# Kernel tuning notes

Hardware: AMD Instinct MI355X
Metric: run time of the kernel (lower is better)

The kernel has to match this reference:

```python
import jax, jax.numpy as jnp
import numpy as np

N_TRAIN, DIM, OUT_DIM, BATCH = 16384, 64, 8, 8192


def setup_inputs() -> dict:
    key = jax.random.key(0)
    k1, k2, k3 = jax.random.split(key, 3)
    batches = jax.random.uniform(k1, (BATCH, DIM), dtype=jnp.float32)
    x_training = jax.random.uniform(k2, (N_TRAIN, DIM), dtype=jnp.float32)
    y_training = jax.random.normal(k3, (N_TRAIN, OUT_DIM), dtype=jnp.float32)
    beta = jnp.ones((1, N_TRAIN), dtype=jnp.float32) / 0.1  # matches ones/0.1 init
    return {"batches": batches, "x_training": x_training,
            "y_training": y_training, "beta": beta}


def reference(batches, x_training, y_training, beta):
    # Pairwise Euclidean distances [batch, n_train] via the expanded form
    # (avoids the O(batch*n_train*dim) repeated tensor the torch code builds).
    b2 = jnp.sum(batches * batches, axis=1, keepdims=True)        # [B, 1]
    x2 = jnp.sum(x_training * x_training, axis=1)[None, :]        # [1, N]
    sq = jnp.maximum(b2 + x2 - 2.0 * (batches @ x_training.T), 0.0)
    dist = jnp.sqrt(sq)                                           # [B, N]
    radial_val = jnp.exp(-beta * dist)                            # RBF kernel [B, N]
    psum1 = jnp.sum(radial_val, axis=1, keepdims=True)            # [B, 1]
    psum2 = radial_val @ y_training                               # [B, OUT_DIM]
    return psum2 / psum1
```

## Files before the change

kernel.cpp:

```cpp
#include <hip/hip_runtime.h>
#include <math.h>
#include <stdint.h>

#define NTRAIN 16384
#define DIM 64
#define ODIM 8
#define BATCH 8192
#define LOG2E 1.4426950408889634f

typedef float f32x16 __attribute__((ext_vector_type(16)));
typedef short short8 __attribute__((ext_vector_type(8)));
typedef _Float16 f16x8 __attribute__((ext_vector_type(8)));
typedef unsigned short u16;

static __device__ __forceinline__ u16 f2bf(float f) {
  unsigned u = __builtin_bit_cast(unsigned, f);
  u += 0x7FFFu + ((u >> 16) & 1u);
  return (u16)(u >> 16);
}
static __device__ __forceinline__ u16 f2h(float f) {
  return __builtin_bit_cast(u16, (_Float16)f);
}
static __device__ __forceinline__ float h2f(u16 h) {
  return (float)__builtin_bit_cast(_Float16, h);
}

static __device__ __forceinline__ f32x16 mfma_bf(short8 a, short8 b, f32x16 c) {
  return __builtin_amdgcn_mfma_f32_32x32x16_bf16(a, b, c, 0, 0, 0);
}
static __device__ __forceinline__ f32x16 mfma_h(f16x8 a, f16x8 b, f32x16 c) {
  return __builtin_amdgcn_mfma_f32_32x32x16_f16(a, b, c, 0, 0, 0);
}
static __device__ __forceinline__ unsigned pkbf(float a, float b) {
  unsigned d;
  asm("v_cvt_pk_bf16_f32 %0, %1, %2" : "=v"(d) : "v"(a), "v"(b));
  return d;
}
static __device__ __forceinline__ float ex2n(float x) {
  float r;
  asm("v_exp_f32 %0, -%1" : "=v"(r) : "v"(x));
  return r;
}
static __device__ __forceinline__ void plswap(unsigned& a, unsigned& b) {
  asm("v_permlane32_swap_b32 %0, %1" : "+v"(a), "+v"(b));
}

__global__ __launch_bounds__(256) void k_norm(
    const float* __restrict__ batches, const float* __restrict__ xt,
    float* __restrict__ b2, float* __restrict__ x2) {
  int i = blockIdx.x * 256 + threadIdx.x;
  if (i >= BATCH + NTRAIN) return;
  const float* row = (i < BATCH) ? batches + (size_t)i * DIM
                                 : xt + (size_t)(i - BATCH) * DIM;
  const float4* r4 = (const float4*)row;
  float s0 = 0.f, s1 = 0.f, s2 = 0.f, s3 = 0.f;
#pragma unroll
  for (int q = 0; q < DIM / 4; ++q) {
    float4 v = r4[q];
    s0 = fmaf(v.x, v.x, s0); s1 = fmaf(v.y, v.y, s1);
    s2 = fmaf(v.z, v.z, s2); s3 = fmaf(v.w, v.w, s3);
  }
  float nrm = (s0 + s1) + (s2 + s3);
  if (i < BATCH) b2[i] = nrm;
  else x2[i - BATCH] = nrm;
}

__global__ __launch_bounds__(256) void k_frag(
    const float* __restrict__ xt, const float* __restrict__ yt,
    const float* __restrict__ beta, const float* __restrict__ x2,
    u16* __restrict__ xf, u16* __restrict__ yv) {
  int tid = blockIdx.x * 256 + threadIdx.x;

  if (tid < (NTRAIN / 32) * 5 * 64) {
    int fg = tid >> 6, lane = tid & 63;
    int tile = fg / 5, f = fg % 5;
    int lr = lane & 31, hi = lane >> 5;
    uint4 u = {0, 0, 0, 0};
    if (f == 4) {
      if (hi == 0) {
        int n = tile * 32 + lr;
        float g = beta[n] * LOG2E;
        float g2v = g * g;
        float gx2v = g2v * x2[n];
        u16 xh = f2h(gx2v);
        u16 xl = f2h(gx2v - h2f(xh));
        u16 gh = f2h(g2v);
        u16 gl = f2h(g2v - h2f(gh));
        u.x = (unsigned)xh | ((unsigned)xl << 16);
        u.y = (unsigned)gh | ((unsigned)gh << 16);
        u.z = (unsigned)gl;
      }
    } else {
      int n = tile * 32 + lr;
      float g = beta[n] * LOG2E;
      float s2g = 2.0f * g * g;
      const float* src = xt + (size_t)n * DIM + f * 16 + hi * 8;
      unsigned e[8];
#pragma unroll
      for (int j = 0; j < 8; ++j) e[j] = f2h(s2g * src[j]);
      u.x = e[0] | (e[1] << 16); u.y = e[2] | (e[3] << 16);
      u.z = e[4] | (e[5] << 16); u.w = e[6] | (e[7] << 16);
    }
    ((uint4*)xf)[(size_t)fg * 64 + lane] = u;
    return;
  }
  tid -= (NTRAIN / 32) * 5 * 64;

  if (tid < (NTRAIN / 16) * 64) {
    int frag = tid >> 6, lane = tid & 63;
    int col = lane & 31, hi = lane >> 5;
    int n = frag * 16 + hi * 8;
    unsigned e[8];
#pragma unroll
    for (int j = 0; j < 8; ++j) {
      float v = (col == 0) ? 1.0f : ((col < 9) ? yt[(size_t)(n + j) * ODIM + (col - 1)] : 0.0f);
      e[j] = f2bf(v);
    }
    uint4 u;
    u.x = e[0] | (e[1] << 16); u.y = e[2] | (e[3] << 16);
    u.z = e[4] | (e[5] << 16); u.w = e[6] | (e[7] << 16);
    ((uint4*)yv)[(size_t)frag * 64 + lane] = u;
  }
}

#define LOAD5(X_, nbv)                                                        \
  {                                                                           \
    const size_t fb_ = (size_t)((nbv) >> 5) * 5;                              \
    _Pragma("unroll")                                                         \
    for (int f = 0; f < 5; ++f) X_[f] = xf4[(fb_ + f) * 64 + lane];           \
  }

#define COMPUTE(X_, nbv)                                                      \
  {                                                                           \
    short8 V0 = __builtin_bit_cast(short8,                                    \
                                   yv4[(size_t)((nbv) >> 4) * 64 + lane]);    \
    short8 V1 = __builtin_bit_cast(                                           \
        short8, yv4[(size_t)((nbv) >> 4) * 64 + 64 + lane]);                  \
    f32x16 sA;                                                                \
    _Pragma("unroll")                                                         \
    for (int r = 0; r < 16; ++r) sA[r] = 0.f;                                 \
    __builtin_amdgcn_s_setprio(1);                                            \
    sA = mfma_h(__builtin_bit_cast(f16x8, X_[4]), AN, sA);                    \
    _Pragma("unroll")                                                         \
    for (int ks = 0; ks < 4; ++ks)                                            \
      sA = mfma_h(__builtin_bit_cast(f16x8, X_[ks]), AH[ks], sA);             \
    __builtin_amdgcn_s_setprio(0);                                            \
    unsigned U[8];                                                            \
    _Pragma("unroll")                                                         \
    for (int p = 0; p < 8; ++p) {                                             \
      float d0 = __builtin_amdgcn_sqrtf(fabsf(sA[2 * p]));                    \
      float d1 = __builtin_amdgcn_sqrtf(fabsf(sA[2 * p + 1]));                \
      U[p] = pkbf(ex2n(d0), ex2n(d1));                                        \
    }                                                                         \
    plswap(U[0], U[2]); plswap(U[1], U[3]);                                   \
    plswap(U[4], U[6]); plswap(U[5], U[7]);                                   \
    uint4 a1 = {U[0], U[1], U[2], U[3]};                                      \
    uint4 a2 = {U[4], U[5], U[6], U[7]};                                      \
    pv = mfma_bf(__builtin_bit_cast(short8, a1), V0, pv);                     \
    pv = mfma_bf(__builtin_bit_cast(short8, a2), V1, pv);                     \
  }

__global__ __launch_bounds__(256, 4) void grnn_pass1(
    const u16* __restrict__ xf, const u16* __restrict__ yv,
    const float* __restrict__ batches, const float* __restrict__ b2,
    float* __restrict__ partial, int chunk_n) {
  const int lane = threadIdx.x & 63;
  const int lr = lane & 31, hi = lane >> 5;
  const int mrow0 = blockIdx.x * 128 + (threadIdx.x >> 6) * 32;
  const int c = blockIdx.y;
  const int n0 = c * chunk_n;
  const int nslab = chunk_n / 32;

  f16x8 AH[4], AN;
  const int mrow = mrow0 + lr;
#pragma unroll
  for (int ks = 0; ks < 4; ++ks) {
    const float* src = batches + (size_t)mrow * DIM + ks * 16 + hi * 8;
    float4 v0 = *(const float4*)src;
    float4 v1 = *(const float4*)(src + 4);
    AH[ks][0] = (_Float16)v0.x; AH[ks][1] = (_Float16)v0.y;
    AH[ks][2] = (_Float16)v0.z; AH[ks][3] = (_Float16)v0.w;
    AH[ks][4] = (_Float16)v1.x; AH[ks][5] = (_Float16)v1.y;
    AH[ks][6] = (_Float16)v1.z; AH[ks][7] = (_Float16)v1.w;
  }
#pragma unroll
  for (int j = 0; j < 8; ++j) AN[j] = (_Float16)0.0f;
  if (hi == 0) {
    float b2v = b2[mrow];
    _Float16 bh = (_Float16)b2v;
    _Float16 bl = (_Float16)(b2v - (float)bh);
    AN[0] = (_Float16)(-1.0f);
    AN[1] = (_Float16)(-1.0f);
    AN[2] = -bh;
    AN[3] = -bl;
    AN[4] = -bh;
  }

  f32x16 pv;
#pragma unroll
  for (int r = 0; r < 16; ++r) pv[r] = 0.f;

  const uint4* xf4 = (const uint4*)xf;
  const uint4* yv4 = (const uint4*)yv;

  uint4 Xa[5], Xb[5];
  LOAD5(Xa, n0)
  for (int s = 0; s < nslab; s += 2) {
    const int nb = n0 + s * 32;
    if (s + 1 < nslab) LOAD5(Xb, nb + 32)
    COMPUTE(Xa, nb)
    if (s + 2 < nslab) LOAD5(Xa, nb + 64)
    if (s + 1 < nslab) COMPUTE(Xb, nb + 32)
  }

  float* pc = partial + (size_t)c * 9 * BATCH;
  if (lr < 9) {
#pragma unroll
    for (int r = 0; r < 16; ++r)
      pc[(size_t)lr * BATCH + (mrow0 + (r & 3) + 8 * (r >> 2) + 4 * hi)] = pv[r];
  }
}

__global__ __launch_bounds__(256) void grnn_pass2(const float* __restrict__ partial,
                                                  float* __restrict__ out, int nc) {
  int b = blockIdx.x * 256 + threadIdx.x;
  float s1 = 0.f;
  float s2[ODIM];
#pragma unroll
  for (int j = 0; j < ODIM; ++j) s2[j] = 0.f;
  for (int cc = 0; cc < nc; ++cc) {
    const float* p = partial + (size_t)cc * 9 * BATCH;
    s1 += p[b];
#pragma unroll
    for (int j = 0; j < ODIM; ++j) s2[j] += p[(size_t)(j + 1) * BATCH + b];
  }
  const float inv = 1.f / s1;
#pragma unroll
  for (int j = 0; j < ODIM; ++j) out[(size_t)b * ODIM + j] = s2[j] * inv;
}

extern "C" void kernel_launch(void* const* d_in, const int* in_sizes, int n_in,
                              void* d_out, int out_size, void* d_ws, size_t ws_size,
                              hipStream_t stream) {
  const float* batches = (const float*)d_in[0];
  const float* xt      = (const float*)d_in[1];
  const float* yt      = (const float*)d_in[2];
  const float* beta    = (const float*)d_in[3];
  float* out = (float*)d_out;

  const size_t xf_b = (size_t)(NTRAIN / 32) * 5 * 1024;
  const size_t yv_b = (size_t)(NTRAIN / 16) * 64 * 16;
  const size_t x2_b = (size_t)NTRAIN * 4;
  const size_t b2_b = (size_t)BATCH * 4;
  const size_t fixed = xf_b + yv_b + x2_b + b2_b;
  const size_t per_chunk = (size_t)9 * BATCH * 4;

  int nc = 32;
  while (nc > 1 && fixed + (size_t)nc * per_chunk > ws_size) nc >>= 1;
  const int chunk_n = NTRAIN / nc;

  char* p = (char*)d_ws;
  u16* xf = (u16*)p;      p += xf_b;
  u16* yv = (u16*)p;      p += yv_b;
  float* x2 = (float*)p;  p += x2_b;
  float* b2 = (float*)p;  p += b2_b;
  float* partial = (float*)p;

  k_norm<<<(BATCH + NTRAIN + 255) / 256, 256, 0, stream>>>(batches, xt, b2, x2);
  const int frag_threads = (NTRAIN / 32) * 5 * 64 + (NTRAIN / 16) * 64;
  k_frag<<<(frag_threads + 255) / 256, 256, 0, stream>>>(xt, yt, beta, x2, xf, yv);
  grnn_pass1<<<dim3(BATCH / 128, nc), 256, 0, stream>>>(
      xf, yv, batches, b2, partial, chunk_n);
  grnn_pass2<<<BATCH / 256, 256, 0, stream>>>(partial, out, nc);
}
```

Baseline: 74.92 us.

## Fuse norm kernel into frag and pass1, remap blocks across XCDs

Drops the separate k_norm launch. Training-row norms are now computed inside k_frag, and batch-row norms inside grnn_pass1 from the values already loaded, combined across half-waves with a permlane swap. The pass1 grid is flattened to 1D with an XCD-aware mapping so that blocks sharing a training chunk land on the same XCD, aiming at better L2 reuse. This saves one launch and some global traffic, at the cost of redundant norm arithmetic in pass1 and extra row reads in k_frag.

```diff
diff --git a/kernel.cpp b/kernel.cpp
--- a/kernel.cpp
+++ b/kernel.cpp
@@ -45,29 +45,9 @@
   asm("v_permlane32_swap_b32 %0, %1" : "+v"(a), "+v"(b));
 }
 
-__global__ __launch_bounds__(256) void k_norm(
-    const float* __restrict__ batches, const float* __restrict__ xt,
-    float* __restrict__ b2, float* __restrict__ x2) {
-  int i = blockIdx.x * 256 + threadIdx.x;
-  if (i >= BATCH + NTRAIN) return;
-  const float* row = (i < BATCH) ? batches + (size_t)i * DIM
-                                 : xt + (size_t)(i - BATCH) * DIM;
-  const float4* r4 = (const float4*)row;
-  float s0 = 0.f, s1 = 0.f, s2 = 0.f, s3 = 0.f;
-#pragma unroll
-  for (int q = 0; q < DIM / 4; ++q) {
-    float4 v = r4[q];
-    s0 = fmaf(v.x, v.x, s0); s1 = fmaf(v.y, v.y, s1);
-    s2 = fmaf(v.z, v.z, s2); s3 = fmaf(v.w, v.w, s3);
-  }
-  float nrm = (s0 + s1) + (s2 + s3);
-  if (i < BATCH) b2[i] = nrm;
-  else x2[i - BATCH] = nrm;
-}
-
 __global__ __launch_bounds__(256) void k_frag(
     const float* __restrict__ xt, const float* __restrict__ yt,
-    const float* __restrict__ beta, const float* __restrict__ x2,
+    const float* __restrict__ beta,
     u16* __restrict__ xf, u16* __restrict__ yv) {
   int tid = blockIdx.x * 256 + threadIdx.x;
 
@@ -81,7 +61,15 @@
         int n = tile * 32 + lr;
         float g = beta[n] * LOG2E;
         float g2v = g * g;
-        float gx2v = g2v * x2[n];
+        const float4* r4 = (const float4*)(xt + (size_t)n * DIM);
+        float s0 = 0.f, s1 = 0.f, s2 = 0.f, s3 = 0.f;
+#pragma unroll
+        for (int q = 0; q < DIM / 4; ++q) {
+          float4 v = r4[q];
+          s0 = fmaf(v.x, v.x, s0); s1 = fmaf(v.y, v.y, s1);
+          s2 = fmaf(v.z, v.z, s2); s3 = fmaf(v.w, v.w, s3);
+        }
+        float gx2v = g2v * ((s0 + s1) + (s2 + s3));
         u16 xh = f2h(gx2v);
         u16 xl = f2h(gx2v - h2f(xh));
         u16 gh = f2h(g2v);
@@ -162,17 +150,29 @@
 
 __global__ __launch_bounds__(256, 4) void grnn_pass1(
     const u16* __restrict__ xf, const u16* __restrict__ yv,
-    const float* __restrict__ batches, const float* __restrict__ b2,
-    float* __restrict__ partial, int chunk_n) {
+    const float* __restrict__ batches,
+    float* __restrict__ partial, int chunk_n, int nc) {
   const int lane = threadIdx.x & 63;
   const int lr = lane & 31, hi = lane >> 5;
-  const int mrow0 = blockIdx.x * 128 + (threadIdx.x >> 6) * 32;
-  const int c = blockIdx.y;
+
+  int mt, c;
+  if (nc == 32) {
+    const int bid = blockIdx.x;
+    const int xcd = bid & 7;
+    const int q = bid >> 3;
+    c = xcd + 8 * (q & 3);
+    mt = q >> 2;
+  } else {
+    mt = blockIdx.x % (BATCH / 128);
+    c = blockIdx.x / (BATCH / 128);
+  }
+  const int mrow0 = mt * 128 + (threadIdx.x >> 6) * 32;
   const int n0 = c * chunk_n;
   const int nslab = chunk_n / 32;
 
   f16x8 AH[4], AN;
   const int mrow = mrow0 + lr;
+  float ssum = 0.f;
 #pragma unroll
   for (int ks = 0; ks < 4; ++ks) {
     const float* src = batches + (size_t)mrow * DIM + ks * 16 + hi * 8;
@@ -182,11 +182,19 @@
     AH[ks][2] = (_Float16)v0.z; AH[ks][3] = (_Float16)v0.w;
     AH[ks][4] = (_Float16)v1.x; AH[ks][5] = (_Float16)v1.y;
     AH[ks][6] = (_Float16)v1.z; AH[ks][7] = (_Float16)v1.w;
-  }
+    ssum = fmaf(v0.x, v0.x, ssum); ssum = fmaf(v0.y, v0.y, ssum);
+    ssum = fmaf(v0.z, v0.z, ssum); ssum = fmaf(v0.w, v0.w, ssum);
+    ssum = fmaf(v1.x, v1.x, ssum); ssum = fmaf(v1.y, v1.y, ssum);
+    ssum = fmaf(v1.z, v1.z, ssum); ssum = fmaf(v1.w, v1.w, ssum);
+  }
+  unsigned ua = __builtin_bit_cast(unsigned, ssum), ub = ua;
+  plswap(ua, ub);
+  const float b2v =
+      __builtin_bit_cast(float, ua) + __builtin_bit_cast(float, ub);
+
 #pragma unroll
   for (int j = 0; j < 8; ++j) AN[j] = (_Float16)0.0f;
   if (hi == 0) {
-    float b2v = b2[mrow];
     _Float16 bh = (_Float16)b2v;
     _Float16 bl = (_Float16)(b2v - (float)bh);
     AN[0] = (_Float16)(-1.0f);
@@ -250,9 +258,7 @@
 
   const size_t xf_b = (size_t)(NTRAIN / 32) * 5 * 1024;
   const size_t yv_b = (size_t)(NTRAIN / 16) * 64 * 16;
-  const size_t x2_b = (size_t)NTRAIN * 4;
-  const size_t b2_b = (size_t)BATCH * 4;
-  const size_t fixed = xf_b + yv_b + x2_b + b2_b;
+  const size_t fixed = xf_b + yv_b;
   const size_t per_chunk = (size_t)9 * BATCH * 4;
 
   int nc = 32;
@@ -262,14 +268,11 @@
   char* p = (char*)d_ws;
   u16* xf = (u16*)p;      p += xf_b;
   u16* yv = (u16*)p;      p += yv_b;
-  float* x2 = (float*)p;  p += x2_b;
-  float* b2 = (float*)p;  p += b2_b;
   float* partial = (float*)p;
 
-  k_norm<<<(BATCH + NTRAIN + 255) / 256, 256, 0, stream>>>(batches, xt, b2, x2);
   const int frag_threads = (NTRAIN / 32) * 5 * 64 + (NTRAIN / 16) * 64;
-  k_frag<<<(frag_threads + 255) / 256, 256, 0, stream>>>(xt, yt, beta, x2, xf, yv);
-  grnn_pass1<<<dim3(BATCH / 128, nc), 256, 0, stream>>>(
-      xf, yv, batches, b2, partial, chunk_n);
+  k_frag<<<(frag_threads + 255) / 256, 256, 0, stream>>>(xt, yt, beta, xf, yv);
+  grnn_pass1<<<(BATCH / 128) * nc, 256, 0, stream>>>(
+      xf, yv, batches, partial, chunk_n, nc);
   grnn_pass2<<<BATCH / 256, 256, 0, stream>>>(partial, out, nc);
 }
```

Measured after the change: 70.56 us. 1.06x faster.
